# Optimization experiments

Hardware: AMD Instinct MI355X
Metric: run time of the kernel (lower is better)

Reference implementation:

```python
import jax, jax.numpy as jnp
import numpy as np

EDGE = 32          # ImageEdge
KPOOL = 16         # pool_kernel_size = ImageEdge // 2
POOLED = 17        # 1 + ImageEdge - pool_kernel_size
NH = 12            # num_attention_heads
HD = 64            # head_dim
HID = 768          # hidden_size
SR = 2             # ScaleRatio


def setup_inputs() -> dict:
    key = jax.random.key(0)
    k1, k2, k3, k4 = jax.random.split(key, 4)
    B, Q = 8, 2048
    return {
        "image_hidden_states": jax.random.normal(k1, (B, EDGE * EDGE, HID), jnp.float32),
        "text_hidden_states": jax.random.normal(k2, (B, Q, HID), jnp.float32),
        "W_in": jax.random.normal(k3, (HID, HID), jnp.float32) * 0.02,   # input_proj (no bias)
        "W_up": jax.random.normal(k4, (HD, HD * SR * SR), jnp.float32) * 0.02,  # up_proj (no bias)
    }


def reference(image_hidden_states, text_hidden_states, W_in, W_up):
    img, txt = image_hidden_states, text_hidden_states
    B, S, HSZ = img.shape            # S = 1024
    Q = txt.shape[1]
    residual = img

    # cross-attention: text queries attend over image keys
    q = txt.reshape(B, Q, NH, HD).transpose(0, 2, 1, 3)   # [B,H,Q,D]
    k = img.reshape(B, S, NH, HD).transpose(0, 2, 1, 3)   # [B,H,S,D]
    attn = jnp.einsum('bhqd,bhkd->bhqk', q, k) / jnp.sqrt(jnp.float32(HD))
    attn = jax.nn.softmax(attn, axis=-1)                  # [B,H,Q,S]
    # dropout is identity in eval mode

    # pooled attention saliency map
    image_attn = attn.sum(axis=2).reshape(B, NH, EDGE, EDGE)
    pooled = jax.lax.reduce_window(
        image_attn, 0.0, jax.lax.add,
        window_dimensions=(1, 1, KPOOL, KPOOL),
        window_strides=(1, 1, 1, 1), padding='VALID') / (KPOOL * KPOOL)   # [B,H,17,17]
    idx = jnp.argmax(pooled.reshape(B, NH, -1), axis=-1)  # [B,H]
    row = (idx // POOLED).reshape(-1)
    col = (idx % POOLED).reshape(-1)

    # gather the argmax-selected 16x16 region per (batch, head)
    states = img.reshape(B, S, NH, HD).transpose(0, 2, 1, 3)
    states = states.reshape(B * NH, EDGE, EDGE, HD)
    slice_one = lambda s, r, c: jax.lax.dynamic_slice(s, (r, c, 0), (KPOOL, KPOOL, HD))
    region = jax.vmap(slice_one)(states, row, col)        # [B*H,16,16,D]

    # pixel-shuffle upsample back to 32x32
    up = region @ W_up                                    # [B*H,16,16,4*D]
    up = up.reshape(B, NH, KPOOL, KPOOL, SR, SR, HD)
    up = up.transpose(0, 1, 2, 4, 3, 5, 6)                # [B,H,16,2,16,2,D]
    up = up.reshape(B, NH, EDGE * EDGE, HD)
    out = up.transpose(0, 2, 1, 3).reshape(B, EDGE * EDGE, HSZ)

    # dense proj + gelu + residual
    out = jax.nn.gelu(out @ W_in, approximate=False)
    return residual + out
```

## Files before the change

kernel.cpp:

```cpp
#include <hip/hip_runtime.h>
#include <cstdint>
#include <cstddef>

#define BB    8
#define NH    12
#define BH    96
#define SS    1024
#define QQ    2048
#define DD    64
#define HID   768
#define EDGE  32
#define KPOOL 16
#define POOLED 17

typedef short bf16x8 __attribute__((ext_vector_type(8)));
typedef _Float16 f16x8 __attribute__((ext_vector_type(8)));
typedef float f32x4  __attribute__((ext_vector_type(4)));

#define MFMA16B(a, b, c) __builtin_amdgcn_mfma_f32_16x16x32_bf16((a), (b), (c), 0, 0, 0)
#define MFMA16H(a, b, c) __builtin_amdgcn_mfma_f32_16x16x32_f16((a), (b), (c), 0, 0, 0)

#define QSCALE 0.18033688011112042f

#if __has_builtin(__builtin_amdgcn_exp2f)
#define EXP2(x) __builtin_amdgcn_exp2f(x)
#else
#define EXP2(x) exp2f(x)
#endif

__device__ __forceinline__ short f2bf(float x) {
    unsigned u = __builtin_bit_cast(unsigned, x);
    u = u + 0x7fffu + ((u >> 16) & 1u);
    return (short)(u >> 16);
}
__device__ __forceinline__ short f2h(float x) {
    _Float16 h = (_Float16)x;
    return __builtin_bit_cast(short, h);
}
__device__ __forceinline__ f16x8 ash(bf16x8 v) {
    return __builtin_bit_cast(f16x8, v);
}


__global__ __launch_bounds__(256) void k_castq(const float* __restrict__ txt,
                                               short* __restrict__ Qs) {
    int i = blockIdx.x * 256 + threadIdx.x;
    int quad = i & 3, kh = (i >> 2) & 1;
    int row = i >> 3;
    int c = row & 15, g = row >> 4;
    int q = row & 2047, bh = row >> 11;
    int b = bh / NH, h = bh - b * NH;
    const float* sp = txt + ((size_t)b * QQ + q) * HID + h * DD + kh * 32 + quad * 8;
    bf16x8 vh, vl;
#pragma unroll
    for (int j = 0; j < 8; j++) {
        float x = sp[j] * QSCALE;
        _Float16 hi = (_Float16)x;
        vh[j] = __builtin_bit_cast(short, hi);
        vl[j] = f2h(x - (float)hi);
    }
    short* dp = Qs + (size_t)g * 2048 + kh * 512 + quad * 128 + c * 8;
    *(bf16x8*)dp = vh;
    *(bf16x8*)(dp + 1024) = vl;
}

__global__ __launch_bounds__(256) void k_castk(const float* __restrict__ img,
                                               short* __restrict__ Ks) {
    int i = blockIdx.x * 256 + threadIdx.x;
    int quad = i & 3, kh = (i >> 2) & 1;
    int row = i >> 3;
    int c = row & 15, g = row >> 4;
    int s = row & 1023, bh = row >> 10;
    int b = bh / NH, h = bh - b * NH;
    const float* sp = img + ((size_t)b * SS + s) * HID + h * DD + kh * 32 + quad * 8;
    bf16x8 vh;
#pragma unroll
    for (int j = 0; j < 8; j++) {
        float x = sp[j];
        _Float16 hi = (_Float16)x;
        vh[j] = __builtin_bit_cast(short, hi);
    }
    short* dp = Ks + (size_t)g * 2048 + kh * 512 + quad * 128 + c * 8;
    *(bf16x8*)dp = vh;
}

__global__ __launch_bounds__(256) void k_castw(const float* __restrict__ W,
                                               const float* __restrict__ Wup,
                                               short* __restrict__ Wt,
                                               short* __restrict__ Wupb) {
    if (blockIdx.x == 144) {
        for (int i = threadIdx.x; i < 16384; i += 256) {
            int k = i >> 8, n = i & 255;
            int addr = (n >> 4) * 1024 + (k >> 5) * 512 + ((k >> 3) & 3) * 128
                     + (n & 15) * 8 + (k & 7);
            Wupb[addr] = f2bf(Wup[k * 256 + n]);
        }
        return;
    }
    __shared__ float T[64][65];
    int bx = blockIdx.x % 12, by = blockIdx.x / 12;
    for (int i = threadIdx.x; i < 4096; i += 256) {
        int r = i >> 6, cc = i & 63;
        T[r][cc] = W[(size_t)(by * 64 + r) * HID + bx * 64 + cc];
    }
    __syncthreads();
    for (int i = threadIdx.x; i < 4096; i += 256) {
        int r = i >> 6, cc = i & 63;
        Wt[(size_t)(bx * 64 + r) * HID + by * 64 + cc] = f2bf(T[cc][r]);
    }
}

__global__ __launch_bounds__(256, 2) void k_lsum(const short* __restrict__ Qs,
                                                 const short* __restrict__ Ks,
                                                 float* __restrict__ Lsum) {
    __shared__ short Kt[2][4096];
    int bh = blockIdx.x % BH;
    int qblk = blockIdx.x / BH;
    int tid = threadIdx.x;
    int w = tid >> 6, lane = tid & 63;
    int quad = lane >> 4, c = lane & 15;

    f16x8 a0[4], a1[4];
    const short* qbase = Qs + (size_t)bh * QQ * 128;
#pragma unroll
    for (int t = 0; t < 4; t++) {
        const short* ap = qbase + (size_t)(qblk * 16 + w * 4 + t) * 2048 + lane * 8;
        a0[t] = ash(*(const bf16x8*)(ap));
        a1[t] = ash(*(const bf16x8*)(ap + 512));
    }
    f32x4 lacc[4];
#pragma unroll
    for (int t = 0; t < 4; t++) lacc[t] = (f32x4){0.f, 0.f, 0.f, 0.f};

    const short* kbase = Ks + (size_t)bh * SS * 128;
    int sg = tid >> 7, so = tid & 127;
    bf16x8 st[2];
#pragma unroll
    for (int j = 0; j < 2; j++)
        st[j] = *(const bf16x8*)(kbase + (size_t)(j * 2 + sg) * 2048 + so * 8);

    for (int t1 = 0; t1 < 16; t1++) {
        int buf = t1 & 1;
#pragma unroll
        for (int j = 0; j < 2; j++)
            *(bf16x8*)(&Kt[buf][j * 2048 + tid * 8]) = st[j];
        if (t1 + 1 < 16) {
#pragma unroll
            for (int j = 0; j < 2; j++)
                st[j] = *(const bf16x8*)(kbase + (size_t)((t1 + 1) * 4 + j * 2 + sg) * 2048 + so * 8);
        }
        __syncthreads();
#pragma unroll
        for (int g = 0; g < 4; g++) {
            const short* kp = &Kt[buf][g * 1024 + lane * 8];
            f16x8 kb0 = ash(*(const bf16x8*)(kp));
            f16x8 kb1 = ash(*(const bf16x8*)(kp + 512));
#pragma unroll
            for (int t = 0; t < 4; t++) {
                f32x4 acc = (f32x4){0.f, 0.f, 0.f, 0.f};
                acc = MFMA16H(a0[t], kb0, acc);
                acc = MFMA16H(a1[t], kb1, acc);
#pragma unroll
                for (int r = 0; r < 4; r++) lacc[t][r] += EXP2(acc[r]);
            }
        }
    }
#pragma unroll
    for (int t = 0; t < 4; t++) {
#pragma unroll
        for (int r = 0; r < 4; r++) {
            float v = lacc[t][r];
            v += __shfl_xor(v, 1);
            v += __shfl_xor(v, 2);
            v += __shfl_xor(v, 4);
            v += __shfl_xor(v, 8);
            if (c == 0)
                Lsum[(size_t)bh * QQ + qblk * 256 + w * 64 + t * 16 + quad * 4 + r] = v;
        }
    }
}

__global__ __launch_bounds__(256, 2) void k_attnacc(const short* __restrict__ Qs,
                                                    const short* __restrict__ Ks,
                                                    const float* __restrict__ Lsum,
                                                    float* __restrict__ iattn) {
    __shared__ short Qt[2][8192];
    int bh = blockIdx.x % BH;
    int rem = blockIdx.x / BH;
    int sblk = rem >> 1, qh = rem & 1;
    int tid = threadIdx.x;
    int w = tid >> 6, lane = tid & 63;
    int quad = lane >> 4, c = lane & 15;

    f16x8 ah0[4], ah1[4];
    const short* kbase = Ks + (size_t)bh * SS * 128;
#pragma unroll
    for (int t = 0; t < 4; t++) {
        const short* ap = kbase + (size_t)(sblk * 16 + w * 4 + t) * 2048 + lane * 8;
        ah0[t] = ash(*(const bf16x8*)(ap));
        ah1[t] = ash(*(const bf16x8*)(ap + 512));
    }
    f32x4 racc[4];
#pragma unroll
    for (int t = 0; t < 4; t++) racc[t] = (f32x4){0.f, 0.f, 0.f, 0.f};

    const short* qbase = Qs + ((size_t)bh * QQ + qh * 1024) * 128;
    const float* lbase = Lsum + (size_t)bh * QQ + qh * 1024;

    bf16x8 st[4];
#pragma unroll
    for (int j = 0; j < 4; j++)
        st[j] = *(const bf16x8*)(qbase + (size_t)j * 2048 + tid * 8);

    for (int t2 = 0; t2 < 16; t2++) {
        int buf = t2 & 1;
#pragma unroll
        for (int j = 0; j < 4; j++)
            *(bf16x8*)(&Qt[buf][j * 2048 + tid * 8]) = st[j];
        if (t2 + 1 < 16) {
#pragma unroll
            for (int j = 0; j < 4; j++)
                st[j] = *(const bf16x8*)(qbase + (size_t)(t2 + 1) * 8192 + j * 2048 + tid * 8);
        }
        __syncthreads();
        float rl[4];
#pragma unroll
        for (int g = 0; g < 4; g++)
            rl[g] = __builtin_amdgcn_rcpf(lbase[t2 * 64 + g * 16 + c]);
#pragma unroll
        for (int g = 0; g < 4; g++) {
            const short* qp = &Qt[buf][g * 2048 + lane * 8];
            f16x8 qb0 = ash(*(const bf16x8*)(qp));
            f16x8 qb1 = ash(*(const bf16x8*)(qp + 512));
            f16x8 qb2 = ash(*(const bf16x8*)(qp + 1024));
            f16x8 qb3 = ash(*(const bf16x8*)(qp + 1536));
#pragma unroll
            for (int t = 0; t < 4; t++) {
                f32x4 acc = (f32x4){0.f, 0.f, 0.f, 0.f};
                acc = MFMA16H(ah0[t], qb0, acc);
                acc = MFMA16H(ah1[t], qb1, acc);
                acc = MFMA16H(ah0[t], qb2, acc);
                acc = MFMA16H(ah1[t], qb3, acc);
#pragma unroll
                for (int r = 0; r < 4; r++)
                    racc[t][r] = fmaf(EXP2(acc[r]), rl[g], racc[t][r]);
            }
        }
    }
#pragma unroll
    for (int t = 0; t < 4; t++) {
#pragma unroll
        for (int r = 0; r < 4; r++) {
            float v = racc[t][r];
            v += __shfl_xor(v, 1);
            v += __shfl_xor(v, 2);
            v += __shfl_xor(v, 4);
            v += __shfl_xor(v, 8);
            if (c == 0)
                atomicAdd(&iattn[(size_t)bh * SS + sblk * 256 + w * 64 + t * 16 + quad * 4 + r], v);
        }
    }
}

__global__ __launch_bounds__(256, 2) void k_up(const float* __restrict__ img,
                                               const float* __restrict__ iattn,
                                               const short* __restrict__ Wupb,
                                               short* __restrict__ Xb) {
    __shared__ short Reg[16384];
    float* F = (float*)Reg;
    float* Apool = F;
    float* Vp = F + 1024;
    float* bvp = F + 1568;
    int*   bip = (int*)(F + 1824);

    int bh = blockIdx.x >> 2, nq = blockIdx.x & 3;
    int b = bh / NH, h = bh - b * NH;
    int tid = threadIdx.x;
    int w = tid >> 6, lane = tid & 63;
    int quad = lane >> 4, c = lane & 15;

    for (int i = tid; i < 1024; i += 256) Apool[i] = iattn[(size_t)bh * SS + i];
    __syncthreads();
    for (int i = tid; i < POOLED * EDGE; i += 256) {
        int r = i >> 5, cc = i & 31;
        float s = 0.f;
#pragma unroll
        for (int k = 0; k < KPOOL; k++) s += Apool[(r + k) * EDGE + cc];
        Vp[i] = s;
    }
    __syncthreads();
    float best = -1e30f;
    int bidx = 1 << 30;
    for (int i = tid; i < POOLED * POOLED; i += 256) {
        int r = i / POOLED, cc = i - r * POOLED;
        float s = 0.f;
#pragma unroll
        for (int k = 0; k < KPOOL; k++) s += Vp[r * EDGE + cc + k];
        if (s > best || (s == best && i < bidx)) { best = s; bidx = i; }
    }
    bvp[tid] = best;
    bip[tid] = bidx;
    __syncthreads();
    for (int off = 128; off; off >>= 1) {
        if (tid < off) {
            float ov = bvp[tid + off];
            int oi = bip[tid + off];
            if (ov > bvp[tid] || (ov == bvp[tid] && oi < bip[tid])) {
                bvp[tid] = ov;
                bip[tid] = oi;
            }
        }
        __syncthreads();
    }
    int widx = bip[0];
    __syncthreads();
    int r0 = widx / POOLED, c0 = widx - r0 * POOLED;

    for (int p = tid; p < 2048; p += 256) {
        int pos = p >> 3, sub = p & 7;
        int gi = r0 + (pos >> 4), gj = c0 + (pos & 15);
        const float* sp = img + ((size_t)b * SS + gi * EDGE + gj) * HID + h * DD + sub * 8;
        bf16x8 v;
#pragma unroll
        for (int j = 0; j < 8; j++) v[j] = f2bf(sp[j]);
        *(bf16x8*)(&Reg[(pos >> 4) * 1024 + (sub >> 2) * 512 + (sub & 3) * 128 + (pos & 15) * 8]) = v;
    }
    __syncthreads();

    bf16x8 bu[4][2];
#pragma unroll
    for (int u = 0; u < 4; u++) {
#pragma unroll
        for (int kh = 0; kh < 2; kh++)
            bu[u][kh] = *(const bf16x8*)(Wupb + (nq * 4 + u) * 1024 + kh * 512 + lane * 8);
    }

#pragma unroll
    for (int t = 0; t < 4; t++) {
        int g = w * 4 + t;
        bf16x8 a0 = *(const bf16x8*)(&Reg[g * 1024 + lane * 8]);
        bf16x8 a1 = *(const bf16x8*)(&Reg[g * 1024 + 512 + lane * 8]);
#pragma unroll
        for (int u = 0; u < 4; u++) {
            f32x4 acc = (f32x4){0.f, 0.f, 0.f, 0.f};
            acc = MFMA16B(a0, bu[u][0], acc);
            acc = MFMA16B(a1, bu[u][1], acc);
#pragma unroll
            for (int r = 0; r < 4; r++) {
                int pos = g * 16 + quad * 4 + r;
                int oc = nq * 64 + u * 16 + c;
                int i16 = pos >> 4, j16 = pos & 15;
                int a = oc >> 7, bbit = (oc >> 6) & 1, dp = oc & 63;
                int p2 = (2 * i16 + a) * EDGE + (2 * j16 + bbit);
                Xb[((size_t)b * SS + p2) * HID + h * DD + dp] = f2bf(acc[r]);
            }
        }
    }
}

__global__ __launch_bounds__(256, 2) void k_out(const short* __restrict__ Xb,
                                                const short* __restrict__ Wt,
                                                const float* __restrict__ img,
                                                float* __restrict__ out) {
    int mblk = blockIdx.x & 63, nblk = blockIdx.x >> 6;
    int wave = threadIdx.x >> 6, lane = threadIdx.x & 63;
    int quad = lane >> 4, c = lane & 15;
    int m0 = mblk * 128 + wave * 32;
    int n0 = nblk * 64;

    f32x4 acc[2][4];
#pragma unroll
    for (int t = 0; t < 2; t++)
#pragma unroll
        for (int u = 0; u < 4; u++) acc[t][u] = (f32x4){0.f, 0.f, 0.f, 0.f};

    for (int k0 = 0; k0 < HID; k0 += 32) {
        bf16x8 a[2], bfr[4];
#pragma unroll
        for (int t = 0; t < 2; t++)
            a[t] = *(const bf16x8*)(Xb + (size_t)(m0 + t * 16 + c) * HID + k0 + quad * 8);
#pragma unroll
        for (int u = 0; u < 4; u++)
            bfr[u] = *(const bf16x8*)(Wt + (size_t)(n0 + u * 16 + c) * HID + k0 + quad * 8);
#pragma unroll
        for (int t = 0; t < 2; t++)
#pragma unroll
            for (int u = 0; u < 4; u++)
                acc[t][u] = MFMA16B(a[t], bfr[u], acc[t][u]);
    }
#pragma unroll
    for (int t = 0; t < 2; t++) {
#pragma unroll
        for (int u = 0; u < 4; u++) {
#pragma unroll
            for (int r = 0; r < 4; r++) {
                int row = m0 + t * 16 + quad * 4 + r;
                int col = n0 + u * 16 + c;
                float x = acc[t][u][r];
                float g = 0.5f * x * (1.f + erff(x * 0.70710678118654752f));
                size_t o = (size_t)row * HID + col;
                out[o] = img[o] + g;
            }
        }
    }
}

extern "C" void kernel_launch(void* const* d_in, const int* in_sizes, int n_in,
                              void* d_out, int out_size, void* d_ws, size_t ws_size,
                              hipStream_t stream) {
    const float* img = (const float*)d_in[0];
    const float* txt = (const float*)d_in[1];
    const float* Win = (const float*)d_in[2];
    const float* Wup = (const float*)d_in[3];
    float* out = (float*)d_out;

    char* w = (char*)d_ws;
    short* Qs    = (short*)(w);
    short* Ks    = (short*)(w + 50331648);
    short* Wt    = (short*)(w + 75497472);
    float* Lsum  = (float*)(w + 76677120);
    float* iattn = (float*)(w + 77463552);
    short* Wupb  = (short*)(w + 77856768);
    short* Xb    = (short*)(w);

    k_castq<<<dim3(6144), dim3(256), 0, stream>>>(txt, Qs);
    k_castk<<<dim3(3072), dim3(256), 0, stream>>>(img, Ks);
    k_castw<<<dim3(145), dim3(256), 0, stream>>>(Win, Wup, Wt, Wupb);
    hipMemsetAsync(iattn, 0, (size_t)BH * SS * sizeof(float), stream);
    k_lsum<<<dim3(768), dim3(256), 0, stream>>>(Qs, Ks, Lsum);
    k_attnacc<<<dim3(768), dim3(256), 0, stream>>>(Qs, Ks, Lsum, iattn);
    k_up<<<dim3(384), dim3(256), 0, stream>>>(img, iattn, Wupb, Xb);
    k_out<<<dim3(768), dim3(256), 0, stream>>>(Xb, Wt, img, out);
}
```

Baseline: 300.5 us.

## Store GEMM operands in MFMA fragment layout and stage k_out through double-buffered LDS

The producer kernels now write Xb and the transposed W_in in a tiled fragment-major layout, so each 16x32 MFMA fragment is one contiguous 1 KB chunk. The output GEMM loads these chunks with coalesced 16-byte loads into double-buffered shared memory, with the next k-slice prefetched into registers, and all waves in the block share the B tile. This targets the strided, uncoalesced global fragment loads of the old k_out and its redundant B reads across waves. In exchange it adds a __syncthreads per k step, uses LDS, and drops the 2-blocks-per-CU launch bound.

```diff
diff --git a/kernel.cpp b/kernel.cpp
--- a/kernel.cpp
+++ b/kernel.cpp
@@ -41,6 +41,11 @@
     return __builtin_bit_cast(f16x8, v);
 }
 
+__device__ __forceinline__ size_t fragaddr(int row, int k) {
+    return ((size_t)(row >> 4) * 24 + (k >> 5)) * 512 + ((k >> 3) & 3) * 128
+         + (row & 15) * 8 + (k & 7);
+}
+
 
 __global__ __launch_bounds__(256) void k_castq(const float* __restrict__ txt,
                                                short* __restrict__ Qs) {
@@ -106,7 +111,8 @@
     __syncthreads();
     for (int i = threadIdx.x; i < 4096; i += 256) {
         int r = i >> 6, cc = i & 63;
-        Wt[(size_t)(bx * 64 + r) * HID + by * 64 + cc] = f2bf(T[cc][r]);
+        int n = bx * 64 + r, k = by * 64 + cc;
+        Wt[fragaddr(n, k)] = f2bf(T[cc][r]);
     }
 }
 
@@ -352,21 +358,30 @@
                 int i16 = pos >> 4, j16 = pos & 15;
                 int a = oc >> 7, bbit = (oc >> 6) & 1, dp = oc & 63;
                 int p2 = (2 * i16 + a) * EDGE + (2 * j16 + bbit);
-                Xb[((size_t)b * SS + p2) * HID + h * DD + dp] = f2bf(acc[r]);
+                int row = b * SS + p2, kdim = h * DD + dp;
+                Xb[fragaddr(row, kdim)] = f2bf(acc[r]);
             }
         }
     }
 }
 
-__global__ __launch_bounds__(256, 2) void k_out(const short* __restrict__ Xb,
-                                                const short* __restrict__ Wt,
-                                                const float* __restrict__ img,
-                                                float* __restrict__ out) {
+__global__ __launch_bounds__(256) void k_out(const short* __restrict__ Xb,
+                                             const short* __restrict__ Wt,
+                                             const float* __restrict__ img,
+                                             float* __restrict__ out) {
+    __shared__ short At[2][4096];
+    __shared__ short Bt[2][2048];
     int mblk = blockIdx.x & 63, nblk = blockIdx.x >> 6;
-    int wave = threadIdx.x >> 6, lane = threadIdx.x & 63;
+    int tid = threadIdx.x;
+    int w = tid >> 6, lane = tid & 63;
     int quad = lane >> 4, c = lane & 15;
-    int m0 = mblk * 128 + wave * 32;
-    int n0 = nblk * 64;
+    int gm0 = mblk * 8, gn0 = nblk * 4;
+    int m0 = mblk * 128, n0 = nblk * 64;
+
+    int ua1 = tid + 256;
+    const short* srcA0 = Xb + ((size_t)(gm0 + (tid >> 6)) * 24) * 512 + (tid & 63) * 8;
+    const short* srcA1 = Xb + ((size_t)(gm0 + (ua1 >> 6)) * 24) * 512 + (ua1 & 63) * 8;
+    const short* srcB  = Wt + ((size_t)(gn0 + (tid >> 6)) * 24) * 512 + (tid & 63) * 8;
 
     f32x4 acc[2][4];
 #pragma unroll
@@ -374,27 +389,44 @@
 #pragma unroll
         for (int u = 0; u < 4; u++) acc[t][u] = (f32x4){0.f, 0.f, 0.f, 0.f};
 
-    for (int k0 = 0; k0 < HID; k0 += 32) {
-        bf16x8 a[2], bfr[4];
-#pragma unroll
-        for (int t = 0; t < 2; t++)
-            a[t] = *(const bf16x8*)(Xb + (size_t)(m0 + t * 16 + c) * HID + k0 + quad * 8);
-#pragma unroll
-        for (int u = 0; u < 4; u++)
-            bfr[u] = *(const bf16x8*)(Wt + (size_t)(n0 + u * 16 + c) * HID + k0 + quad * 8);
-#pragma unroll
-        for (int t = 0; t < 2; t++)
-#pragma unroll
-            for (int u = 0; u < 4; u++)
-                acc[t][u] = MFMA16B(a[t], bfr[u], acc[t][u]);
-    }
+    bf16x8 sa0 = *(const bf16x8*)(srcA0);
+    bf16x8 sa1 = *(const bf16x8*)(srcA1);
+    bf16x8 sb  = *(const bf16x8*)(srcB);
+
+    for (int kk = 0; kk < 24; kk++) {
+        int buf = kk & 1;
+        *(bf16x8*)(&At[buf][tid * 8]) = sa0;
+        *(bf16x8*)(&At[buf][ua1 * 8]) = sa1;
+        *(bf16x8*)(&Bt[buf][tid * 8]) = sb;
+        if (kk + 1 < 24) {
+            sa0 = *(const bf16x8*)(srcA0 + (kk + 1) * 512);
+            sa1 = *(const bf16x8*)(srcA1 + (kk + 1) * 512);
+            sb  = *(const bf16x8*)(srcB  + (kk + 1) * 512);
+        }
+        __syncthreads();
+        bf16x8 a0 = *(const bf16x8*)(&At[buf][(2 * w + 0) * 512 + lane * 8]);
+        bf16x8 a1 = *(const bf16x8*)(&At[buf][(2 * w + 1) * 512 + lane * 8]);
+        bf16x8 b0 = *(const bf16x8*)(&Bt[buf][0 * 512 + lane * 8]);
+        bf16x8 b1 = *(const bf16x8*)(&Bt[buf][1 * 512 + lane * 8]);
+        bf16x8 b2 = *(const bf16x8*)(&Bt[buf][2 * 512 + lane * 8]);
+        bf16x8 b3 = *(const bf16x8*)(&Bt[buf][3 * 512 + lane * 8]);
+        acc[0][0] = MFMA16B(a0, b0, acc[0][0]);
+        acc[0][1] = MFMA16B(a0, b1, acc[0][1]);
+        acc[0][2] = MFMA16B(a0, b2, acc[0][2]);
+        acc[0][3] = MFMA16B(a0, b3, acc[0][3]);
+        acc[1][0] = MFMA16B(a1, b0, acc[1][0]);
+        acc[1][1] = MFMA16B(a1, b1, acc[1][1]);
+        acc[1][2] = MFMA16B(a1, b2, acc[1][2]);
+        acc[1][3] = MFMA16B(a1, b3, acc[1][3]);
+    }
+
 #pragma unroll
     for (int t = 0; t < 2; t++) {
 #pragma unroll
         for (int u = 0; u < 4; u++) {
 #pragma unroll
             for (int r = 0; r < 4; r++) {
-                int row = m0 + t * 16 + quad * 4 + r;
+                int row = m0 + w * 32 + t * 16 + quad * 4 + r;
                 int col = n0 + u * 16 + c;
                 float x = acc[t][u][r];
                 float g = 0.5f * x * (1.f + erff(x * 0.70710678118654752f));
```

Measured after the change: 272.1 us. 9.5% less time.
